# Kernel optimization log

Measured on AMD Instinct MI355X. Metric: run time of the kernel, lower is better.

The kernel has to match this reference:

```python
import jax, jax.numpy as jnp
import numpy as np

DIM = 1024
N_HEAD = 16
HEAD_DIM = DIM // N_HEAD
SCALE = HEAD_DIM ** (-0.5)


def setup_inputs() -> dict:
    key = jax.random.key(0)
    ks = jax.random.split(key, 5)
    x = jax.random.normal(ks[0], (2, 2048, DIM), dtype=jnp.float32)
    # Linear params (torch nn.Linear stores weight as [out, in]; we keep [in, out])
    wqkv = jax.random.normal(ks[1], (DIM, 3 * DIM), dtype=jnp.float32) / np.sqrt(DIM)
    bqkv = jax.random.normal(ks[2], (3 * DIM,), dtype=jnp.float32) * 0.01
    wo = jax.random.normal(ks[3], (DIM, DIM), dtype=jnp.float32) / np.sqrt(DIM)
    bo = jax.random.normal(ks[4], (DIM,), dtype=jnp.float32) * 0.01
    return {"x": x, "wqkv": wqkv, "bqkv": bqkv, "wo": wo, "bo": bo}


def reference(x, wqkv, bqkv, wo, bo):
    b, s, _ = x.shape
    qkv = x @ wqkv + bqkv                      # [b, s, 3*dim]
    q, k, v = jnp.split(qkv, 3, axis=-1)
    # [b, s, h, d] -> [b, h, s, d]
    def heads(t):
        return t.reshape(b, s, N_HEAD, HEAD_DIM).transpose(0, 2, 1, 3)
    q, k, v = heads(q) * SCALE, heads(k), heads(v)
    attn = jnp.einsum('bhqd,bhkd->bhqk', q, k)  # [b, h, s, s]
    attn = jax.nn.softmax(attn, axis=-1)
    out = jnp.einsum('bhqk,bhkd->bhqd', attn, v)
    out = out.transpose(0, 2, 1, 3).reshape(b, s, DIM)
    return out @ wo + bo
```

## Files before the change

### kernel.cpp

```cpp
#include <hip/hip_runtime.h>
#include <hip/hip_bf16.h>

#define DIM   1024
#define NHEAD 16
#define HDIM  64
#define BATCH 2
#define SEQ   2048
#define TOK   (BATCH*SEQ)
#define QSCALE 0.1803368801111204f

typedef unsigned short u16;
typedef __attribute__((ext_vector_type(8))) _Float16 h16x8;
typedef __attribute__((ext_vector_type(2))) __fp16 fp16x2;
typedef __attribute__((ext_vector_type(4))) float f32x4;
typedef __attribute__((ext_vector_type(16))) float f32x16;
typedef __attribute__((ext_vector_type(2))) int i32x2;

__device__ __forceinline__ u16 f2h(float f) {
    union { _Float16 h; u16 u; } v; v.h = (_Float16)f;
    return v.u;
}
__device__ __forceinline__ unsigned pack2h(float a, float b) {
    return (unsigned)f2h(a) | ((unsigned)f2h(b) << 16);
}
__device__ __forceinline__ unsigned pkrtz(float a, float b) {
    union { fp16x2 h; unsigned u; } v;
    v.h = __builtin_amdgcn_cvt_pkrtz(a, b);
    return v.u;
}
__device__ __forceinline__ f32x16 zero16() {
    f32x16 v;
#pragma unroll
    for (int i = 0; i < 16; ++i) v[i] = 0.f;
    return v;
}

typedef __attribute__((address_space(3))) void lds_void;
typedef const __attribute__((address_space(1))) void gbl_void;
__device__ __forceinline__ void gload_lds16(const void* g, void* l) {
    __builtin_amdgcn_global_load_lds((gbl_void*)g, (lds_void*)l, 16, 0, 0);
}

__global__ __launch_bounds__(256)
void fused_cvt(const float* __restrict__ x,    u16* __restrict__ xh,
               const float* __restrict__ wqkv, u16* __restrict__ wqT,
               const float* __restrict__ wo,   u16* __restrict__ woT) {
    __shared__ float t[32][33];
    const int bid = blockIdx.x;
    if (bid < 4096) {
        int i = bid * 256 + threadIdx.x;
        float4 v = ((const float4*)x)[i];
        ((uint2*)xh)[i] = make_uint2(pack2h(v.x, v.y), pack2h(v.z, v.w));
        return;
    }
    const float* in; u16* outT; int K, N, tb;
    if (bid < 7168) { in = wqkv; outT = wqT; K = 1024; N = 3072; tb = bid - 4096; }
    else            { in = wo;   outT = woT; K = 1024; N = 1024; tb = bid - 7168; }
    const int nbx = N / 32;
    const int n0 = (tb % nbx) * 32, k0 = (tb / nbx) * 32;
    const int tx = threadIdx.x & 31, ty = threadIdx.x >> 5;
#pragma unroll
    for (int i = 0; i < 4; ++i)
        t[ty + i * 8][tx] = in[(size_t)(k0 + ty + i * 8) * N + n0 + tx];
    __syncthreads();
#pragma unroll
    for (int i = 0; i < 4; ++i)
        outT[(size_t)(n0 + ty + i * 8) * K + k0 + tx] = f2h(t[tx][ty + i * 8]);
}

__global__ __launch_bounds__(256)
void gemm_qkv(const u16* __restrict__ Ag, const u16* __restrict__ Bg,
              const float* __restrict__ bias, u16* __restrict__ Qh,
              u16* __restrict__ Kh, u16* __restrict__ Vh, int K, int N) {
    __shared__ u16 As[128 * 64];
    __shared__ u16 Bs[128 * 64];

    const int tid  = threadIdx.x;
    const int lane = tid & 63;
    const int w    = tid >> 6;
    const int c    = lane & 15;
    const int quad = lane >> 4;
    const int wm   = (w & 1) * 64;
    const int wn   = (w >> 1) * 64;
    const int row0 = blockIdx.y * 128;
    const int col0 = blockIdx.x * 128;
    const int sw   = c & 7;

    f32x4 acc[4][4];
#pragma unroll
    for (int m = 0; m < 4; ++m)
#pragma unroll
        for (int n = 0; n < 4; ++n) acc[m][n] = (f32x4){0.f, 0.f, 0.f, 0.f};

    for (int k0 = 0; k0 < K; k0 += 64) {
        __syncthreads();
#pragma unroll
        for (int i = 0; i < 4; ++i) {
            int idx = tid + i * 256;
            int r = idx >> 3, p = idx & 7;
            int g = p ^ (r & 7);
            gload_lds16(Ag + (size_t)(row0 + r) * K + k0 + g * 8, &As[idx * 8]);
            gload_lds16(Bg + (size_t)(col0 + r) * K + k0 + g * 8, &Bs[idx * 8]);
        }
        __syncthreads();

        h16x8 af[4][2];
#pragma unroll
        for (int m = 0; m < 4; ++m)
#pragma unroll
            for (int kh = 0; kh < 2; ++kh)
                af[m][kh] = *(const h16x8*)&As[(wm + m * 16 + c) * 64 +
                                              ((kh * 4 + quad) ^ sw) * 8];
#pragma unroll
        for (int kh = 0; kh < 2; ++kh)
#pragma unroll
            for (int n = 0; n < 4; ++n) {
                h16x8 bf = *(const h16x8*)&Bs[(wn + n * 16 + c) * 64 +
                                              ((kh * 4 + quad) ^ sw) * 8];
#pragma unroll
                for (int m = 0; m < 4; ++m)
                    acc[m][n] = __builtin_amdgcn_mfma_f32_16x16x32_f16(
                        af[m][kh], bf, acc[m][n], 0, 0, 0);
            }
    }

#pragma unroll
    for (int n = 0; n < 4; ++n) {
        const int col = col0 + wn + n * 16 + c;
        const float bv = bias[col];
        const int h = (col >> 6) & 15, d = col & 63;
#pragma unroll
        for (int m = 0; m < 4; ++m) {
            const int rbase = row0 + wm + m * 16 + quad * 4;
            const int b = rbase >> 11, s0 = rbase & (SEQ - 1);
            const int bh = (b << 4) + h;
            if (col0 < DIM) {
#pragma unroll
                for (int r = 0; r < 4; ++r)
                    Qh[((size_t)bh * SEQ + s0 + r) * 64 + d] =
                        f2h((acc[m][n][r] + bv) * QSCALE);
            } else if (col0 < 2 * DIM) {
#pragma unroll
                for (int r = 0; r < 4; ++r)
                    Kh[((size_t)bh * SEQ + s0 + r) * 64 + d] =
                        f2h(acc[m][n][r] + bv);
            } else {
                uint2 pv = make_uint2(pack2h(acc[m][n][0] + bv, acc[m][n][1] + bv),
                                      pack2h(acc[m][n][2] + bv, acc[m][n][3] + bv));
                *(uint2*)&Vh[((size_t)bh * 64 + d) * SEQ + s0] = pv;
            }
        }
    }
}

__global__ __launch_bounds__(256)
void gemm_out(const u16* __restrict__ Ag, const u16* __restrict__ Bg,
              const float* __restrict__ bias, float* __restrict__ Cout,
              int M, int N, int K) {
    __shared__ u16 As[128 * 64];
    __shared__ u16 Bs[128 * 64];

    const int tid  = threadIdx.x;
    const int lane = tid & 63;
    const int w    = tid >> 6;
    const int c    = lane & 15;
    const int quad = lane >> 4;
    const int wm   = (w & 1) * 64;
    const int wn   = (w >> 1) * 64;
    const int row0 = blockIdx.y * 128;
    const int col0 = blockIdx.x * 128;
    const int sw   = c & 7;

    f32x4 acc[4][4];
#pragma unroll
    for (int m = 0; m < 4; ++m)
#pragma unroll
        for (int n = 0; n < 4; ++n) acc[m][n] = (f32x4){0.f, 0.f, 0.f, 0.f};

    for (int k0 = 0; k0 < K; k0 += 64) {
        __syncthreads();
#pragma unroll
        for (int i = 0; i < 4; ++i) {
            int idx = tid + i * 256;
            int r = idx >> 3, p = idx & 7;
            int g = p ^ (r & 7);
            gload_lds16(Ag + (size_t)(row0 + r) * K + k0 + g * 8, &As[idx * 8]);
            gload_lds16(Bg + (size_t)(col0 + r) * K + k0 + g * 8, &Bs[idx * 8]);
        }
        __syncthreads();

        h16x8 af[4][2];
#pragma unroll
        for (int m = 0; m < 4; ++m)
#pragma unroll
            for (int kh = 0; kh < 2; ++kh)
                af[m][kh] = *(const h16x8*)&As[(wm + m * 16 + c) * 64 +
                                              ((kh * 4 + quad) ^ sw) * 8];
#pragma unroll
        for (int kh = 0; kh < 2; ++kh)
#pragma unroll
            for (int n = 0; n < 4; ++n) {
                h16x8 bf = *(const h16x8*)&Bs[(wn + n * 16 + c) * 64 +
                                              ((kh * 4 + quad) ^ sw) * 8];
#pragma unroll
                for (int m = 0; m < 4; ++m)
                    acc[m][n] = __builtin_amdgcn_mfma_f32_16x16x32_f16(
                        af[m][kh], bf, acc[m][n], 0, 0, 0);
            }
    }

#pragma unroll
    for (int n = 0; n < 4; ++n) {
        const int col = col0 + wn + n * 16 + c;
        const float bv = bias[col];
#pragma unroll
        for (int m = 0; m < 4; ++m) {
            const int rbase = row0 + wm + m * 16 + quad * 4;
#pragma unroll
            for (int r = 0; r < 4; ++r)
                Cout[(size_t)(rbase + r) * N + col] = acc[m][n][r] + bv;
        }
    }
}

__global__ __launch_bounds__(256, 2)
void flash_attn11(const u16* __restrict__ Qg, const u16* __restrict__ Kg,
                  const u16* __restrict__ Vg, u16* __restrict__ aout) {
    __shared__ u16 Qs[128 * 64];
    __shared__ u16 Ks[2][128 * 64];
    __shared__ u16 Vt[2][64 * 128];

    const int tid  = threadIdx.x;
    const int lane = tid & 63;
    const int w    = tid >> 6;
    const int wq   = w & 1;
    const int wk   = w >> 1;
    const int n32  = lane & 31;
    const int q5   = lane >> 5;
    const int bh   = blockIdx.y;
    const int q0   = blockIdx.x * 128;

    const u16* Qb = Qg + (size_t)bh * SEQ * 64;
    const u16* Kb = Kg + (size_t)bh * SEQ * 64;
    const u16* Vb = Vg + (size_t)bh * 64 * SEQ;

#pragma unroll
    for (int i = 0; i < 4; ++i) {
        int idx = tid + i * 256;
        int r = idx >> 3, p = idx & 7, g = p ^ (r & 7);
        gload_lds16(Qb + (size_t)(q0 + r) * 64 + g * 8, &Qs[idx * 8]);
    }
#pragma unroll
    for (int i = 0; i < 4; ++i) {
        int idx = tid + i * 256;
        int rk = idx >> 3, pk = idx & 7, gk = pk ^ (rk & 7);
        gload_lds16(Kb + (size_t)rk * 64 + gk * 8, &Ks[0][idx * 8]);
        int rv = idx >> 4, cv = idx & 15, gv = cv ^ (rv & 7);
        gload_lds16(Vb + (size_t)rv * SEQ + gv * 8, &Vt[0][idx * 8]);
    }
    __syncthreads();

    const int qrowA = wq * 64 + n32;
    const int qrowB = qrowA + 32;
    const int sw    = n32 & 7;
    h16x8 qbA[4], qbB[4];
#pragma unroll
    for (int s = 0; s < 4; ++s) {
        const int ch = ((s * 2 + q5) ^ sw) * 8;
        qbA[s] = *(const h16x8*)&Qs[qrowA * 64 + ch];
        qbB[s] = *(const h16x8*)&Qs[qrowB * 64 + ch];
    }

    float lA = 0.f, lB = 0.f;
    f32x16 oA[2] = {zero16(), zero16()};
    f32x16 oB[2] = {zero16(), zero16()};

    for (int kt = 0; kt < SEQ / 128; ++kt) {
        const int cur = kt & 1, nxt = cur ^ 1;

        if (kt < SEQ / 128 - 1) {
            const int k1 = (kt + 1) * 128;
#pragma unroll
            for (int i = 0; i < 4; ++i) {
                int idx = tid + i * 256;
                int rk = idx >> 3, pk = idx & 7, gk = pk ^ (rk & 7);
                gload_lds16(Kb + (size_t)(k1 + rk) * 64 + gk * 8, &Ks[nxt][idx * 8]);
                int rv = idx >> 4, cv = idx & 15, gv = cv ^ (rv & 7);
                gload_lds16(Vb + (size_t)rv * SEQ + k1 + gv * 8, &Vt[nxt][idx * 8]);
            }
        }

        unsigned xwA[8][2], xwB[8][2];
#pragma unroll
        for (int sub = 0; sub < 2; ++sub) {
            const int kr = wk * 64 + sub * 32 + n32;
            f32x16 saA = zero16(), saB = zero16();
            __builtin_amdgcn_s_setprio(1);
#pragma unroll
            for (int s = 0; s < 4; ++s) {
                h16x8 ak = *(const h16x8*)&Ks[cur][kr * 64 +
                                                   (((s * 2 + q5) ^ sw) * 8)];
                saA = __builtin_amdgcn_mfma_f32_32x32x16_f16(ak, qbA[s], saA, 0, 0, 0);
                saB = __builtin_amdgcn_mfma_f32_32x32x16_f16(ak, qbB[s], saB, 0, 0, 0);
            }
            __builtin_amdgcn_s_setprio(0);
#pragma unroll
            for (int rr = 0; rr < 4; ++rr) {
                float a0 = __builtin_amdgcn_exp2f(saA[4 * rr + 0]);
                float a1 = __builtin_amdgcn_exp2f(saA[4 * rr + 1]);
                float a2 = __builtin_amdgcn_exp2f(saA[4 * rr + 2]);
                float a3 = __builtin_amdgcn_exp2f(saA[4 * rr + 3]);
                lA += (a0 + a1) + (a2 + a3);
                xwA[sub * 4 + rr][0] = pkrtz(a0, a1);
                xwA[sub * 4 + rr][1] = pkrtz(a2, a3);
                float b0 = __builtin_amdgcn_exp2f(saB[4 * rr + 0]);
                float b1 = __builtin_amdgcn_exp2f(saB[4 * rr + 1]);
                float b2 = __builtin_amdgcn_exp2f(saB[4 * rr + 2]);
                float b3 = __builtin_amdgcn_exp2f(saB[4 * rr + 3]);
                lB += (b0 + b1) + (b2 + b3);
                xwB[sub * 4 + rr][0] = pkrtz(b0, b1);
                xwB[sub * 4 + rr][1] = pkrtz(b2, b3);
            }
        }

        h16x8 bpA[4], bpB[4];
#pragma unroll
        for (int s = 0; s < 4; ++s) {
            i32x2 ra = __builtin_amdgcn_permlane32_swap(
                (int)xwA[2 * s][0], (int)xwA[2 * s + 1][0], false, false);
            i32x2 rb = __builtin_amdgcn_permlane32_swap(
                (int)xwA[2 * s][1], (int)xwA[2 * s + 1][1], false, false);
            union { int u[4]; h16x8 h; } fa;
            fa.u[0] = ra[0]; fa.u[1] = rb[0]; fa.u[2] = ra[1]; fa.u[3] = rb[1];
            bpA[s] = fa.h;
            i32x2 rc = __builtin_amdgcn_permlane32_swap(
                (int)xwB[2 * s][0], (int)xwB[2 * s + 1][0], false, false);
            i32x2 rd = __builtin_amdgcn_permlane32_swap(
                (int)xwB[2 * s][1], (int)xwB[2 * s + 1][1], false, false);
            union { int u[4]; h16x8 h; } fb;
            fb.u[0] = rc[0]; fb.u[1] = rd[0]; fb.u[2] = rc[1]; fb.u[3] = rd[1];
            bpB[s] = fb.h;
        }

        __builtin_amdgcn_s_setprio(1);
#pragma unroll
        for (int dt = 0; dt < 2; ++dt) {
            const int dr = dt * 32 + n32;
#pragma unroll
            for (int s = 0; s < 4; ++s) {
                h16x8 av = *(const h16x8*)&Vt[cur][dr * 128 +
                                                   ((wk * 8 + ((s * 2 + q5) ^ sw)) * 8)];
                oA[dt] = __builtin_amdgcn_mfma_f32_32x32x16_f16(av, bpA[s], oA[dt], 0, 0, 0);
                oB[dt] = __builtin_amdgcn_mfma_f32_32x32x16_f16(av, bpB[s], oB[dt], 0, 0, 0);
            }
        }
        __builtin_amdgcn_s_setprio(0);

        __syncthreads();
    }

    lA += __shfl_xor(lA, 32, 64);
    lB += __shfl_xor(lB, 32, 64);

    float* oc = (float*)Vt;
    float* lc = (float*)Qs;
    const int rowA = (wq * 2 + 0) * 64 + lane;
    const int rowB = (wq * 2 + 1) * 64 + lane;
    if (wk == 1) {
#pragma unroll
        for (int dt = 0; dt < 2; ++dt)
#pragma unroll
            for (int i = 0; i < 16; ++i) {
                oc[rowA * 32 + ((dt * 16 + i + lane) & 31)] = oA[dt][i];
                oc[rowB * 32 + ((dt * 16 + i + lane) & 31)] = oB[dt][i];
            }
        lc[rowA] = lA;
        lc[rowB] = lB;
    }
    __syncthreads();
    if (wk == 1) return;
    lA += lc[rowA];
    lB += lc[rowB];
#pragma unroll
    for (int dt = 0; dt < 2; ++dt)
#pragma unroll
        for (int i = 0; i < 16; ++i) {
            oA[dt][i] += oc[rowA * 32 + ((dt * 16 + i + lane) & 31)];
            oB[dt][i] += oc[rowB * 32 + ((dt * 16 + i + lane) & 31)];
        }

    const float invA = 1.f / lA, invB = 1.f / lB;
    const int b = bh >> 4, h = bh & 15;
    const size_t roA = (size_t)(b * SEQ + q0 + qrowA) * DIM + h * HDIM;
    const size_t roB = (size_t)(b * SEQ + q0 + qrowB) * DIM + h * HDIM;
#pragma unroll
    for (int dt = 0; dt < 2; ++dt) {
#pragma unroll
        for (int rq = 0; rq < 4; ++rq) {
            const int d = dt * 32 + 8 * rq + 4 * q5;
            *(uint2*)&aout[roA + d] = make_uint2(
                pkrtz(oA[dt][4 * rq + 0] * invA, oA[dt][4 * rq + 1] * invA),
                pkrtz(oA[dt][4 * rq + 2] * invA, oA[dt][4 * rq + 3] * invA));
            *(uint2*)&aout[roB + d] = make_uint2(
                pkrtz(oB[dt][4 * rq + 0] * invB, oB[dt][4 * rq + 1] * invB),
                pkrtz(oB[dt][4 * rq + 2] * invB, oB[dt][4 * rq + 3] * invB));
        }
    }
}

extern "C" void kernel_launch(void* const* d_in, const int* in_sizes, int n_in,
                              void* d_out, int out_size, void* d_ws, size_t ws_size,
                              hipStream_t stream) {
    (void)in_sizes; (void)n_in; (void)out_size; (void)ws_size;
    const float* x    = (const float*)d_in[0];
    const float* wqkv = (const float*)d_in[1];
    const float* bqkv = (const float*)d_in[2];
    const float* wo   = (const float*)d_in[3];
    const float* bo   = (const float*)d_in[4];
    float* out = (float*)d_out;

    const size_t HB = (size_t)BATCH * NHEAD * SEQ * HDIM;
    u16* Qh  = (u16*)d_ws;
    u16* Kh  = Qh + HB;
    u16* Vh  = Kh + HB;
    u16* ao  = Vh + HB;
    u16* wqT = ao + (size_t)TOK * DIM;
    u16* woT = wqT + (size_t)3 * DIM * DIM;
    u16* xh  = woT + (size_t)DIM * DIM;

    fused_cvt<<<8192, 256, 0, stream>>>(x, xh, wqkv, wqT, wo, woT);
    gemm_qkv<<<dim3(3 * DIM / 128, TOK / 128), 256, 0, stream>>>(
        xh, wqT, bqkv, Qh, Kh, Vh, DIM, 3 * DIM);
    flash_attn11<<<dim3(SEQ / 128, BATCH * NHEAD), 256, 0, stream>>>(
        Qh, Kh, Vh, ao);
    gemm_out<<<dim3(DIM / 128, TOK / 128), 256, 0, stream>>>(
        ao, woT, bo, out, TOK, DIM, DIM);
}
```

Measured before the change: 185.3 us.

## Single-buffer K/V and load Q directly to registers to raise attention occupancy

```diff
diff --git a/kernel.cpp b/kernel.cpp
--- a/kernel.cpp
+++ b/kernel.cpp
@@ -223,12 +223,14 @@
     }
 }
 
-__global__ __launch_bounds__(256, 2)
-void flash_attn11(const u16* __restrict__ Qg, const u16* __restrict__ Kg,
+__global__ __launch_bounds__(256, 4)
+void flash_attn13(const u16* __restrict__ Qg, const u16* __restrict__ Kg,
                   const u16* __restrict__ Vg, u16* __restrict__ aout) {
-    __shared__ u16 Qs[128 * 64];
-    __shared__ u16 Ks[2][128 * 64];
-    __shared__ u16 Vt[2][64 * 128];
+    __shared__ u16 KV[2][64 * 128];
+    __shared__ float lc[256];
+
+    u16* Ks = KV[0];
+    u16* Vt = KV[1];
 
     const int tid  = threadIdx.x;
     const int lane = tid & 63;
@@ -244,31 +246,19 @@
     const u16* Kb = Kg + (size_t)bh * SEQ * 64;
     const u16* Vb = Vg + (size_t)bh * 64 * SEQ;
 
-#pragma unroll
-    for (int i = 0; i < 4; ++i) {
-        int idx = tid + i * 256;
-        int r = idx >> 3, p = idx & 7, g = p ^ (r & 7);
-        gload_lds16(Qb + (size_t)(q0 + r) * 64 + g * 8, &Qs[idx * 8]);
-    }
-#pragma unroll
-    for (int i = 0; i < 4; ++i) {
-        int idx = tid + i * 256;
-        int rk = idx >> 3, pk = idx & 7, gk = pk ^ (rk & 7);
-        gload_lds16(Kb + (size_t)rk * 64 + gk * 8, &Ks[0][idx * 8]);
-        int rv = idx >> 4, cv = idx & 15, gv = cv ^ (rv & 7);
-        gload_lds16(Vb + (size_t)rv * SEQ + gv * 8, &Vt[0][idx * 8]);
-    }
-    __syncthreads();
-
     const int qrowA = wq * 64 + n32;
     const int qrowB = qrowA + 32;
     const int sw    = n32 & 7;
+
     h16x8 qbA[4], qbB[4];
-#pragma unroll
-    for (int s = 0; s < 4; ++s) {
-        const int ch = ((s * 2 + q5) ^ sw) * 8;
-        qbA[s] = *(const h16x8*)&Qs[qrowA * 64 + ch];
-        qbB[s] = *(const h16x8*)&Qs[qrowB * 64 + ch];
+    {
+        const u16* qa  = Qb + (size_t)(q0 + qrowA) * 64;
+        const u16* qb_ = Qb + (size_t)(q0 + qrowB) * 64;
+#pragma unroll
+        for (int s = 0; s < 4; ++s) {
+            qbA[s] = *(const h16x8*)&qa[(s * 2 + q5) * 8];
+            qbB[s] = *(const h16x8*)&qb_[(s * 2 + q5) * 8];
+        }
     }
 
     float lA = 0.f, lB = 0.f;
@@ -276,19 +266,19 @@
     f32x16 oB[2] = {zero16(), zero16()};
 
     for (int kt = 0; kt < SEQ / 128; ++kt) {
-        const int cur = kt & 1, nxt = cur ^ 1;
-
-        if (kt < SEQ / 128 - 1) {
-            const int k1 = (kt + 1) * 128;
-#pragma unroll
-            for (int i = 0; i < 4; ++i) {
-                int idx = tid + i * 256;
-                int rk = idx >> 3, pk = idx & 7, gk = pk ^ (rk & 7);
-                gload_lds16(Kb + (size_t)(k1 + rk) * 64 + gk * 8, &Ks[nxt][idx * 8]);
-                int rv = idx >> 4, cv = idx & 15, gv = cv ^ (rv & 7);
-                gload_lds16(Vb + (size_t)rv * SEQ + k1 + gv * 8, &Vt[nxt][idx * 8]);
-            }
-        }
+        const int k1 = kt * 128;
+
+        if (kt) __syncthreads();
+
+#pragma unroll
+        for (int i = 0; i < 4; ++i) {
+            int idx = tid + i * 256;
+            int rk = idx >> 3, pk = idx & 7, gk = pk ^ (rk & 7);
+            gload_lds16(Kb + (size_t)(k1 + rk) * 64 + gk * 8, &Ks[idx * 8]);
+            int rv = idx >> 4, cv = idx & 15, gv = cv ^ (rv & 7);
+            gload_lds16(Vb + (size_t)rv * SEQ + k1 + gv * 8, &Vt[idx * 8]);
+        }
+        __syncthreads();
 
         unsigned xwA[8][2], xwB[8][2];
 #pragma unroll
@@ -298,8 +288,8 @@
             __builtin_amdgcn_s_setprio(1);
 #pragma unroll
             for (int s = 0; s < 4; ++s) {
-                h16x8 ak = *(const h16x8*)&Ks[cur][kr * 64 +
-                                                   (((s * 2 + q5) ^ sw) * 8)];
+                h16x8 ak = *(const h16x8*)&Ks[kr * 64 +
+                                              (((s * 2 + q5) ^ sw) * 8)];
                 saA = __builtin_amdgcn_mfma_f32_32x32x16_f16(ak, qbA[s], saA, 0, 0, 0);
                 saB = __builtin_amdgcn_mfma_f32_32x32x16_f16(ak, qbB[s], saB, 0, 0, 0);
             }
@@ -348,22 +338,20 @@
             const int dr = dt * 32 + n32;
 #pragma unroll
             for (int s = 0; s < 4; ++s) {
-                h16x8 av = *(const h16x8*)&Vt[cur][dr * 128 +
-                                                   ((wk * 8 + ((s * 2 + q5) ^ sw)) * 8)];
+                h16x8 av = *(const h16x8*)&Vt[dr * 128 +
+                                              ((wk * 8 + ((s * 2 + q5) ^ sw)) * 8)];
                 oA[dt] = __builtin_amdgcn_mfma_f32_32x32x16_f16(av, bpA[s], oA[dt], 0, 0, 0);
                 oB[dt] = __builtin_amdgcn_mfma_f32_32x32x16_f16(av, bpB[s], oB[dt], 0, 0, 0);
             }
         }
         __builtin_amdgcn_s_setprio(0);
-
-        __syncthreads();
-    }
+    }
+    __syncthreads();
 
     lA += __shfl_xor(lA, 32, 64);
     lB += __shfl_xor(lB, 32, 64);
 
-    float* oc = (float*)Vt;
-    float* lc = (float*)Qs;
+    float* oc = (float*)KV;
     const int rowA = (wq * 2 + 0) * 64 + lane;
     const int rowB = (wq * 2 + 1) * 64 + lane;
     if (wk == 1) {
@@ -431,7 +419,7 @@
     fused_cvt<<<8192, 256, 0, stream>>>(x, xh, wqkv, wqT, wo, woT);
     gemm_qkv<<<dim3(3 * DIM / 128, TOK / 128), 256, 0, stream>>>(
         xh, wqT, bqkv, Qh, Kh, Vh, DIM, 3 * DIM);
-    flash_attn11<<<dim3(SEQ / 128, BATCH * NHEAD), 256, 0, stream>>>(
+    flash_attn13<<<dim3(SEQ / 128, BATCH * NHEAD), 256, 0, stream>>>(
         Qh, Kh, Vh, ao);
     gemm_out<<<dim3(DIM / 128, TOK / 128), 256, 0, stream>>>(
         ao, woT, bo, out, TOK, DIM, DIM);
```

Result: slower. 606.6 us (+227.3%).
